# Optimization experiments

Hardware: AMD Instinct MI355X
Metric: run time of the kernel (lower is better)

Reference implementation:

```python
import jax, jax.numpy as jnp
import numpy as np

N = 65536      # nodes
E = 1048576    # edges (avg degree 16)
L = 24         # input_length == lstm input size == lstm num_layers
H = 64         # lstm hidden


def _lin_init(key, fi, fo):
    return jax.random.normal(key, (fi, fo), jnp.float32) / np.sqrt(fi)


def setup_inputs() -> dict:
    key = jax.random.key(0)
    ks = iter(jax.random.split(key, 64))
    d = {}
    d["x"] = jax.random.normal(next(ks), (N, 421 + L), jnp.float32)
    d["edge_index"] = jax.random.randint(next(ks), (2, E), 0, N)

    def lin(fi, fo):
        return _lin_init(next(ks), fi, fo), jnp.zeros((fo,), jnp.float32)

    d["poi1_W"], d["poi1_b"] = lin(13, 64)
    d["poi2_W"], d["poi2_b"] = lin(64, 64)
    d["svi1_W"], d["svi1_b"] = lin(365, 128)
    d["svi2_W"], d["svi2_b"] = lin(128, 128)
    d["all1_W"], d["all1_b"] = lin(192, 128)
    d["all2_W"], d["all2_b"] = lin(128, 128)
    for name, fi, fo in (("gat1", 128, 128), ("gat2", 128, 128), ("gat3", 128, 64)):
        d[name + "_W"], d[name + "_b"] = lin(fi, fo)
        d[name + "_asrc"] = jax.random.normal(next(ks), (fo,), jnp.float32) / np.sqrt(fo)
        d[name + "_adst"] = jax.random.normal(next(ks), (fo,), jnp.float32) / np.sqrt(fo)
    d["lstm_Wih0"] = jax.random.normal(next(ks), (L, 4 * H), jnp.float32) / np.sqrt(L)
    d["lstm_Wih"] = jax.random.normal(next(ks), (L - 1, H, 4 * H), jnp.float32) / np.sqrt(H)
    d["lstm_Whh"] = jax.random.normal(next(ks), (L, H, 4 * H), jnp.float32) / np.sqrt(H)
    d["lstm_b"] = jnp.zeros((L, 4 * H), jnp.float32)
    d["time1_W"], d["time1_b"] = lin(64, 64)
    d["time2_W"], d["time2_b"] = lin(64, 64)
    d["lin1_W"], d["lin1_b"] = lin(128, 64)
    d["lin2_W"], d["lin2_b"] = lin(64, 64)
    d["lin3_W"], d["lin3_b"] = lin(64, 1)
    return d


def _gat(h_in, W, a_src, a_dst, b, src, dst, n):
    # PyG GATConv (1 head): gather -> per-edge attn -> segment softmax -> scatter
    h = h_in @ W                                   # [N, F]
    s = h @ a_src                                  # [N]
    t = h @ a_dst                                  # [N]
    e = jax.nn.leaky_relu(s[src] + t[dst], 0.2)    # [E']
    m = jax.ops.segment_max(e, dst, num_segments=n)
    ee = jnp.exp(e - m[dst])
    denom = jax.ops.segment_sum(ee, dst, num_segments=n)
    alpha = ee / denom[dst]
    out = jax.ops.segment_sum(h[src] * alpha[:, None], dst, num_segments=n)
    return out + b


def _forward(x, poi1_W, poi1_b, poi2_W, poi2_b, svi1_W, svi1_b, svi2_W, svi2_b,
             all1_W, all1_b, all2_W, all2_b,
             gat1_W, gat1_b, gat1_asrc, gat1_adst,
             gat2_W, gat2_b, gat2_asrc, gat2_adst,
             gat3_W, gat3_b, gat3_asrc, gat3_adst,
             lstm_Wih0, lstm_Wih, lstm_Whh, lstm_b,
             time1_W, time1_b, time2_W, time2_b,
             lin1_W, lin1_b, lin2_W, lin2_b, lin3_W, lin3_b,
             edge_index):
    n = x.shape[0]
    relu = jax.nn.relu
    # feature-branch MLPs
    x_poi = relu(relu(x[:, 3:16] @ poi1_W + poi1_b) @ poi2_W + poi2_b)
    x_svi = relu(relu(x[:, 56:421] @ svi1_W + svi1_b) @ svi2_W + svi2_b)
    h = jnp.concatenate([x_poi, x_svi], axis=1)
    h = relu(relu(h @ all1_W + all1_b) @ all2_W + all2_b)
    # add self loops once (PyG GATConv default add_self_loops=True)
    loops = jnp.arange(n, dtype=edge_index.dtype)
    src = jnp.concatenate([edge_index[0], loops])
    dst = jnp.concatenate([edge_index[1], loops])
    h = relu(_gat(h, gat1_W, gat1_asrc, gat1_adst, gat1_b, src, dst, n))
    h = relu(_gat(h, gat2_W, gat2_asrc, gat2_adst, gat2_b, src, dst, n))
    h = relu(_gat(h, gat3_W, gat3_asrc, gat3_adst, gat3_b, src, dst, n))
    # stacked LSTM over the single timestep t (h0=c0=0 -> f gate & Whh contribute 0)
    inp = x[:, 421:]                               # [N, L]
    hs = []
    for l in range(L):
        Wih = lstm_Wih0 if l == 0 else lstm_Wih[l - 1]
        gates = inp @ Wih + lstm_b[l]              # [N, 4H], torch gate order i,f,g,o
        i, f, g, o = jnp.split(gates, 4, axis=-1)
        c = jax.nn.sigmoid(i) * jnp.tanh(g)
        h_l = jax.nn.sigmoid(o) * jnp.tanh(c)
        hs.append(h_l)
        inp = h_l
    t = hs[2]                                      # hn[2]
    t = relu(relu(t @ time1_W + time1_b) @ time2_W + time2_b)
    z = jnp.concatenate([h, t], axis=1)            # [N, 128]
    z = relu(z @ lin1_W + lin1_b)
    z = relu(z @ lin2_W + lin2_b)
    return z @ lin3_W + lin3_b                     # [N, 1]


def reference(x, edge_index, poi1_W, poi1_b, poi2_W, poi2_b, svi1_W, svi1_b,
              svi2_W, svi2_b, all1_W, all1_b, all2_W, all2_b,
              gat1_W, gat1_b, gat1_asrc, gat1_adst,
              gat2_W, gat2_b, gat2_asrc, gat2_adst,
              gat3_W, gat3_b, gat3_asrc, gat3_adst,
              lstm_Wih0, lstm_Wih, lstm_Whh, lstm_b,
              time1_W, time1_b, time2_W, time2_b,
              lin1_W, lin1_b, lin2_W, lin2_b, lin3_W, lin3_b):
    return _forward(x, poi1_W, poi1_b, poi2_W, poi2_b, svi1_W, svi1_b, svi2_W, svi2_b,
                    all1_W, all1_b, all2_W, all2_b,
                    gat1_W, gat1_b, gat1_asrc, gat1_adst,
                    gat2_W, gat2_b, gat2_asrc, gat2_adst,
                    gat3_W, gat3_b, gat3_asrc, gat3_adst,
                    lstm_Wih0, lstm_Wih, lstm_Whh, lstm_b,
                    time1_W, time1_b, time2_W, time2_b,
                    lin1_W, lin1_b, lin2_W, lin2_b, lin3_W, lin3_b,
                    edge_index)
```

## Files before the change

kernel.cpp:

```cpp
#include <hip/hip_runtime.h>
#include <math.h>

#define DEV __device__ __forceinline__

typedef __attribute__((ext_vector_type(8))) short short8;
typedef __attribute__((ext_vector_type(4))) float f32x4;
typedef float f32x4u __attribute__((ext_vector_type(4), aligned(4)));
typedef __attribute__((ext_vector_type(4))) unsigned int u32x4;
typedef __attribute__((ext_vector_type(4))) _Float16 h16x4;

#define NEG_BIG (-3.0e38f)
#define CAPB 4096
#define CHUNK 4096

DEV float sigm(float x) { return 1.0f / (1.0f + __expf(-x)); }
DEV float leaky(float e) { return (e >= 0.0f) ? e : 0.2f * e; }

DEV void split_bf16(const float f[8], short8& hi, short8& lo) {
#pragma unroll
  for (int i = 0; i < 8; ++i) {
    unsigned u = __builtin_bit_cast(unsigned, f[i]);
    hi[i] = (short)(u >> 16);
    float h = __builtin_bit_cast(float, u & 0xffff0000u);
    float r = f[i] - h;
    lo[i] = (short)(__builtin_bit_cast(unsigned, r) >> 16);
  }
}

DEV unsigned packsplit(float v) {
  unsigned u = __builtin_bit_cast(unsigned, v);
  unsigned hf = u & 0xffff0000u;
  float r = v - __builtin_bit_cast(float, hf);
  return hf | (__builtin_bit_cast(unsigned, r) >> 16);
}

DEV void unpack_pk(const u32x4 p0, const u32x4 p1, short8& hi, short8& lo) {
  u32x4 h, l;
  h[0] = __builtin_amdgcn_perm(p0[1], p0[0], 0x07060302u);
  h[1] = __builtin_amdgcn_perm(p0[3], p0[2], 0x07060302u);
  h[2] = __builtin_amdgcn_perm(p1[1], p1[0], 0x07060302u);
  h[3] = __builtin_amdgcn_perm(p1[3], p1[2], 0x07060302u);
  l[0] = __builtin_amdgcn_perm(p0[1], p0[0], 0x05040100u);
  l[1] = __builtin_amdgcn_perm(p0[3], p0[2], 0x05040100u);
  l[2] = __builtin_amdgcn_perm(p1[1], p1[0], 0x05040100u);
  l[3] = __builtin_amdgcn_perm(p1[3], p1[2], 0x05040100u);
  hi = __builtin_bit_cast(short8, h);
  lo = __builtin_bit_cast(short8, l);
}

template <int G, int MT, int NT>
DEV void mfma_grp(f32x4 (&acc)[MT][NT], const short8 (&ah)[MT],
                  const short8 (&al)[MT], const short8 (&bh)[4],
                  const short8 (&bl)[4]) {
#pragma unroll
  for (int mt = 0; mt < MT; ++mt)
#pragma unroll
    for (int j = 0; j < 4; ++j) {
      acc[mt][G * 4 + j] = __builtin_amdgcn_mfma_f32_16x16x32_bf16(
          ah[mt], bh[j], acc[mt][G * 4 + j], 0, 0, 0);
      acc[mt][G * 4 + j] = __builtin_amdgcn_mfma_f32_16x16x32_bf16(
          ah[mt], bl[j], acc[mt][G * 4 + j], 0, 0, 0);
      acc[mt][G * 4 + j] = __builtin_amdgcn_mfma_f32_16x16x32_bf16(
          al[mt], bh[j], acc[mt][G * 4 + j], 0, 0, 0);
    }
}


__global__ void fill_i32_kernel(int* p, int v, int n) {
  int i = blockIdx.x * blockDim.x + threadIdx.x;
  if (i < n) p[i] = v;
}


__global__ __launch_bounds__(256) void bucket_bin(
    const int* __restrict__ ei, int* __restrict__ bucket_cnt,
    unsigned* __restrict__ ebuf, int E, int Et) {
  __shared__ unsigned stage[CHUNK];
  __shared__ int hist[512], rbase[512], lcur[512];
  const int tid = threadIdx.x;
  const long long e0 = (long long)blockIdx.x * CHUNK;
  const int nalive = (int)((Et - e0) < CHUNK ? (Et - e0) : CHUNK);
  for (int i = tid; i < 512; i += 256) hist[i] = 0;
  __syncthreads();
  for (int k = tid; k < nalive; k += 256) {
    long long e = e0 + k;
    int s, d;
    if (e < E) { s = ei[e]; d = ei[E + e]; } else { s = (int)(e - E); d = s; }
    unsigned p = (unsigned)s | ((unsigned)d << 16);
    stage[k] = p;
    atomicAdd(&hist[d >> 7], 1);
  }
  __syncthreads();
  for (int i = tid; i < 512; i += 256) {
    int c = hist[i];
    rbase[i] = c ? atomicAdd(&bucket_cnt[i], c) : 0;
    lcur[i] = 0;
  }
  __syncthreads();
  for (int k = tid; k < nalive; k += 256) {
    unsigned p = stage[k];
    int b = (int)(p >> 23);
    int lofs = atomicAdd(&lcur[b], 1);
    int pos = rbase[b] + lofs;
    if (pos < CAPB) ebuf[(long long)b * CAPB + pos] = p;
  }
}

__global__ __launch_bounds__(512) void bucket_scan(
    const int* __restrict__ cnt, int* __restrict__ start, int Et) {
  __shared__ int sh[512];
  int tid = threadIdx.x;
  int v = cnt[tid];
  sh[tid] = v;
  __syncthreads();
  int val = v;
  for (int off = 1; off < 512; off <<= 1) {
    int add = (tid >= off) ? sh[tid - off] : 0;
    __syncthreads();
    val += add;
    sh[tid] = val;
    __syncthreads();
  }
  start[tid] = val - v;
  if (tid == 511) start[512] = Et;
}

__global__ __launch_bounds__(128) void bucket_csr(
    const unsigned* __restrict__ ebuf, const int* __restrict__ bucket_cnt,
    const int* __restrict__ bucket_start, int* __restrict__ row_start,
    int* __restrict__ srcs, int N, int Et) {
  __shared__ unsigned stage[CAPB];
  __shared__ int hist[128], hbase[128], lcur[128];
  const int b = blockIdx.x, tid = threadIdx.x;
  int cnt = bucket_cnt[b];
  cnt = cnt < CAPB ? cnt : CAPB;
  const int gbase = bucket_start[b];
  hist[tid] = 0;
  __syncthreads();
  const unsigned* eb = ebuf + (long long)b * CAPB;
  for (int k = tid; k < cnt; k += 128) {
    unsigned p = eb[k];
    stage[k] = p;
    atomicAdd(&hist[(p >> 16) & 127], 1);
  }
  __syncthreads();
  int v = hist[tid];
  hbase[tid] = v;
  __syncthreads();
  int val = v;
  for (int off = 1; off < 128; off <<= 1) {
    int add = (tid >= off) ? hbase[tid - off] : 0;
    __syncthreads();
    val += add;
    hbase[tid] = val;
    __syncthreads();
  }
  int ex = val - v;
  row_start[b * 128 + tid] = gbase + ex;
  __syncthreads();
  hbase[tid] = ex;
  lcur[tid] = 0;
  __syncthreads();
  for (int k = tid; k < cnt; k += 128) {
    unsigned p = stage[k];
    int o = (p >> 16) & 127;
    int lofs = atomicAdd(&lcur[o], 1);
    srcs[gbase + hbase[o] + lofs] = (int)(p & 0xffffu);
  }
  if (b == 0 && tid == 0) row_start[N] = Et;
}

struct WJobs {
  const float* W[16];
  short* hi[16];
  short* lo[16];
  int K[16];
  int M16[16];
  int ldw[16];
  int skip[16];
  int tile0[16];
};

__global__ __launch_bounds__(64) void wsplit_all(WJobs jb, int njobs) {
  int b = blockIdx.x;
  int ji = 0;
#pragma unroll
  for (int i = 1; i < 16; ++i)
    if (i < njobs && b >= jb.tile0[i]) ji = i;
  int t = b - jb.tile0[ji];
  int M16 = jb.M16[ji];
  int kc = t / M16, ntG = t % M16;
  int K = jb.K[ji], ldw = jb.ldw[ji];
  const float* __restrict__ W = jb.W[ji];

  int lane = threadIdx.x;
  int kb = kc * 32 + (lane >> 4) * 8;
  int c = ntG * 16 + (lane & 15);
  if (jb.skip[ji] && c >= 64) c += 64;
  float f[8];
#pragma unroll
  for (int j = 0; j < 8; ++j) {
    int k = kb + j;
    f[j] = (k < K) ? W[(long long)k * ldw + c] : 0.0f;
  }
  short8 h, l;
  split_bf16(f, h, l);
  long long off = ((long long)t * 64 + lane) * 8;
  *(short8*)(jb.hi[ji] + off) = h;
  *(short8*)(jb.lo[ji] + off) = l;
}


struct GemmArgs {
  const void* A; const short* wh; const short* wl; const float* bias;
  void* C; const float* asrc; const float* adst; float* sOut; float* tOut;
  int lda, ldc, K, KC, act;
};

struct LstmArgs {
  const void* A; const short* wh; const short* wl; const float* bias;
  unsigned* H; int lda, K, KC;
};

template <int MT, int NT, int APK, int OPK, int STE>
DEV void gemm_body(const GemmArgs& g, int bid) {
  const int lane = threadIdx.x;
  const int m = lane & 15, q = lane >> 4;
  const long long r0 = (long long)bid * (MT * 16);
  const int K = g.K, KC = g.KC, lda = g.lda;

  f32x4 acc[MT][NT];
#pragma unroll
  for (int i = 0; i < MT; ++i)
#pragma unroll
    for (int j = 0; j < NT; ++j) acc[i][j] = (f32x4)(0.0f);

  u32x4 pA[MT][2];
  float fA[MT][8];

  auto loadA = [&](int kc) {
#pragma unroll
    for (int mt = 0; mt < MT; ++mt) {
      if (APK == 1) {
        const unsigned* ap =
            (const unsigned*)g.A + (r0 + mt * 16 + m) * lda + kc * 32 + q * 8;
        pA[mt][0] = *(const u32x4*)ap;
        pA[mt][1] = *(const u32x4*)(ap + 4);
      } else {
        const float* ap =
            (const float*)g.A + (r0 + mt * 16 + m) * lda + kc * 32 + q * 8;
        if (kc * 32 + 32 <= K) {
          f32x4u p0 = *(const f32x4u*)ap;
          f32x4u p1 = *(const f32x4u*)(ap + 4);
#pragma unroll
          for (int j = 0; j < 4; ++j) { fA[mt][j] = p0[j]; fA[mt][4 + j] = p1[j]; }
        } else {
#pragma unroll
          for (int j = 0; j < 8; ++j) {
            int k = kc * 32 + q * 8 + j;
            fA[mt][j] = (k < K) ? ap[j] : 0.0f;
          }
        }
      }
    }
  };

  short8 ah[MT], al[MT];
  auto unpackA = [&]() {
#pragma unroll
    for (int mt = 0; mt < MT; ++mt) {
      if (APK == 1)
        unpack_pk(pA[mt][0], pA[mt][1], ah[mt], al[mt]);
      else
        split_bf16(fA[mt], ah[mt], al[mt]);
    }
  };

  short8 bh0[4], bl0[4], bh1[4], bl1[4];
  auto loadB = [&](short8 (&bh)[4], short8 (&bl)[4], int kc, int gg) {
#pragma unroll
    for (int j = 0; j < 4; ++j) {
      long long off = (((long long)kc * NT + (gg * 4 + j)) * 64 + lane) * 8;
      bh[j] = *(const short8*)(g.wh + off);
      bl[j] = *(const short8*)(g.wl + off);
    }
  };

  if constexpr (NT == 4) {
    loadA(0);
    loadB(bh0, bl0, 0, 0);
    int kc = 0;
    for (; kc + 2 <= KC; kc += 2) {
      unpackA();
      loadB(bh1, bl1, kc + 1, 0);
      loadA(kc + 1);
      mfma_grp<0, MT, NT>(acc, ah, al, bh0, bl0);
      unpackA();
      if (kc + 2 < KC) {
        loadB(bh0, bl0, kc + 2, 0);
        loadA(kc + 2);
      }
      mfma_grp<0, MT, NT>(acc, ah, al, bh1, bl1);
    }
    if (kc < KC) {
      unpackA();
      mfma_grp<0, MT, NT>(acc, ah, al, bh0, bl0);
    }
  } else {
    loadA(0);
    loadB(bh0, bl0, 0, 0);
    for (int kc = 0; kc < KC; ++kc) {
      unpackA();
      loadB(bh1, bl1, kc, 1);
      if (kc + 1 < KC) loadA(kc + 1);
      mfma_grp<0, MT, NT>(acc, ah, al, bh0, bl0);
      if (kc + 1 < KC) loadB(bh0, bl0, kc + 1, 0);
      mfma_grp<1, MT, NT>(acc, ah, al, bh1, bl1);
    }
  }

  if (STE == 2) {
    float w3[NT], bs[NT];
#pragma unroll
    for (int nt = 0; nt < NT; ++nt) {
      int col = nt * 16 + m;
      w3[nt] = g.asrc[col];
      bs[nt] = g.bias[col];
    }
#pragma unroll
    for (int mt = 0; mt < MT; ++mt)
#pragma unroll
      for (int reg = 0; reg < 4; ++reg) {
        float ps = 0.0f;
#pragma unroll
        for (int nt = 0; nt < NT; ++nt) {
          float v = fmaxf(acc[mt][nt][reg] + bs[nt], 0.0f);
          ps = fmaf(v, w3[nt], ps);
        }
#pragma unroll
        for (int off = 1; off < 16; off <<= 1) ps += __shfl_xor(ps, off, 64);
        if (m == 0) g.sOut[r0 + mt * 16 + q * 4 + reg] = ps + g.adst[0];
      }
    return;
  }

#pragma unroll
  for (int nt = 0; nt < NT; ++nt) {
    int col = nt * 16 + m;
    float bsv = g.bias ? g.bias[col] : 0.0f;
#pragma unroll
    for (int mt = 0; mt < MT; ++mt) {
      long long rb = r0 + mt * 16 + q * 4;
#pragma unroll
      for (int reg = 0; reg < 4; ++reg) {
        float v = acc[mt][nt][reg] + bsv;
        if (g.act == 1) v = fmaxf(v, 0.0f);
        if (OPK == 1)
          ((unsigned*)g.C)[(rb + reg) * g.ldc + col] = packsplit(v);
        else if (OPK == 2)
          ((_Float16*)g.C)[(rb + reg) * g.ldc + col] = (_Float16)v;
        else
          ((float*)g.C)[(rb + reg) * g.ldc + col] = v;
      }
    }
  }

  if (STE == 1) {
    float as[NT], ad[NT];
#pragma unroll
    for (int nt = 0; nt < NT; ++nt) {
      int col = nt * 16 + m;
      as[nt] = g.asrc[col];
      ad[nt] = g.adst[col];
    }
#pragma unroll
    for (int mt = 0; mt < MT; ++mt)
#pragma unroll
      for (int reg = 0; reg < 4; ++reg) {
        float ps = 0.0f, pt = 0.0f;
#pragma unroll
        for (int nt = 0; nt < NT; ++nt) {
          ps = fmaf(acc[mt][nt][reg], as[nt], ps);
          pt = fmaf(acc[mt][nt][reg], ad[nt], pt);
        }
#pragma unroll
        for (int off = 1; off < 16; off <<= 1) {
          ps += __shfl_xor(ps, off, 64);
          pt += __shfl_xor(pt, off, 64);
        }
        if (m == 0) {
          long long r = r0 + mt * 16 + q * 4 + reg;
          g.sOut[r] = ps;
          g.tOut[r] = pt;
        }
      }
  }
}

template <int APK>
DEV void lstm_body(const LstmArgs& g, int bid) {
  const int lane = threadIdx.x;
  const int m = lane & 15, q = lane >> 4;
  const long long r0 = (long long)bid * 16;
  const int K = g.K, KC = g.KC, lda = g.lda;

  f32x4 acc[12];
#pragma unroll
  for (int j = 0; j < 12; ++j) acc[j] = (f32x4)(0.0f);

  u32x4 pA[2];
  float fA[8];

  auto loadA = [&](int kc) {
    if (APK == 1) {
      const unsigned* ap = (const unsigned*)g.A + (r0 + m) * lda + kc * 32 + q * 8;
      pA[0] = *(const u32x4*)ap;
      pA[1] = *(const u32x4*)(ap + 4);
    } else {
      const float* ap = (const float*)g.A + (r0 + m) * lda + kc * 32 + q * 8;
      if (kc * 32 + 32 <= K) {
        f32x4u p0 = *(const f32x4u*)ap;
        f32x4u p1 = *(const f32x4u*)(ap + 4);
#pragma unroll
        for (int j = 0; j < 4; ++j) { fA[j] = p0[j]; fA[4 + j] = p1[j]; }
      } else {
#pragma unroll
        for (int j = 0; j < 8; ++j) {
          int k = kc * 32 + q * 8 + j;
          fA[j] = (k < K) ? ap[j] : 0.0f;
        }
      }
    }
  };

  short8 bh0, bl0, bh1, bl1;
  auto loadB = [&](short8& bh, short8& bl, int kc, int nt) {
    long long off = (((long long)kc * 12 + nt) * 64 + lane) * 8;
    bh = *(const short8*)(g.wh + off);
    bl = *(const short8*)(g.wl + off);
  };

  loadA(0);
  loadB(bh0, bl0, 0, 0);
  for (int kc = 0; kc < KC; ++kc) {
    short8 ah, al;
    if (APK == 1)
      unpack_pk(pA[0], pA[1], ah, al);
    else
      split_bf16(fA, ah, al);
    loadB(bh1, bl1, kc, 1);
    if (kc + 1 < KC) loadA(kc + 1);
    const int kn = (kc + 1 < KC) ? kc + 1 : kc;
#pragma unroll
    for (int nt = 0; nt < 12; ++nt) {
      short8& cbh = (nt & 1) ? bh1 : bh0;
      short8& cbl = (nt & 1) ? bl1 : bl0;
      acc[nt] = __builtin_amdgcn_mfma_f32_16x16x32_bf16(ah, cbh, acc[nt], 0, 0, 0);
      acc[nt] = __builtin_amdgcn_mfma_f32_16x16x32_bf16(ah, cbl, acc[nt], 0, 0, 0);
      acc[nt] = __builtin_amdgcn_mfma_f32_16x16x32_bf16(al, cbh, acc[nt], 0, 0, 0);
      if (nt + 2 < 12)
        loadB((nt & 1) ? bh1 : bh0, (nt & 1) ? bl1 : bl0, kc, nt + 2);
      else if (nt + 2 == 12)
        loadB(bh0, bl0, kn, 0);
    }
  }

#pragma unroll
  for (int nt = 0; nt < 4; ++nt) {
    int col = nt * 16 + m;
    float bi = g.bias[col], bg = g.bias[128 + col], bo = g.bias[192 + col];
#pragma unroll
    for (int reg = 0; reg < 4; ++reg) {
      float gi = acc[nt][reg] + bi;
      float gg = acc[nt + 4][reg] + bg;
      float go = acc[nt + 8][reg] + bo;
      float cc = sigm(gi) * tanhf(gg);
      g.H[(r0 + q * 4 + reg) * 64 + col] = packsplit(sigm(go) * tanhf(cc));
    }
  }
}


template <int MT, int NT, int APK, int OPK, int STE>
__global__ __launch_bounds__(64) void gemm_mfma(GemmArgs g) {
  gemm_body<MT, NT, APK, OPK, STE>(g, blockIdx.x);
}

template <int NTa, int APKa, int OPKa, int STEa,
          int NTb, int APKb, int OPKb, int STEb>
__global__ __launch_bounds__(64) void combo_gg(GemmArgs a, GemmArgs b, int nA) {
  int bid = blockIdx.x;
  if (bid < nA)
    gemm_body<2, NTa, APKa, OPKa, STEa>(a, bid);
  else
    gemm_body<2, NTb, APKb, OPKb, STEb>(b, bid - nA);
}

template <int NTa, int APKa, int OPKa, int STEa, int LAPK>
__global__ __launch_bounds__(64) void combo_gl(GemmArgs a, LstmArgs l, int nA) {
  int bid = blockIdx.x;
  if (bid < nA)
    gemm_body<2, NTa, APKa, OPKa, STEa>(a, bid);
  else
    lstm_body<LAPK>(l, bid - nA);
}

template <int NTa, int APKa, int OPKa, int STEa,
          int NTb, int APKb, int OPKb, int STEb, int LAPK>
__global__ __launch_bounds__(64) void combo_ggl(GemmArgs a, GemmArgs b,
                                                LstmArgs l, int nA, int nAB) {
  int bid = blockIdx.x;
  if (bid < nA)
    gemm_body<2, NTa, APKa, OPKa, STEa>(a, bid);
  else if (bid < nAB)
    gemm_body<2, NTb, APKb, OPKb, STEb>(b, bid - nA);
  else
    lstm_body<LAPK>(l, bid - nAB);
}


template <int FO, int OPK>
__global__ __launch_bounds__(256) void gat_agg(
    const _Float16* __restrict__ G, const float* __restrict__ s,
    const float* __restrict__ t, const int* __restrict__ row_start,
    const int* __restrict__ srcs, const float* __restrict__ bias,
    void* __restrict__ outv, int ldc) {
  constexpr int CAP = 128;
  constexpr int LPE = FO / 4;
  constexpr int EPW = 64 / LPE;
  __shared__ float ecache[4][CAP];
  __shared__ int icache[4][CAP];
  const int wv = threadIdx.x >> 6;
  const int lane = threadIdx.x & 63;
  const int d = blockIdx.x * 4 + wv;
  const int start = row_start[d], end = row_start[d + 1];
  const float td = t[d];

  float m = NEG_BIG, dsum = 0.0f;
  for (int j = start + lane; j < end; j += 64) {
    int sj = srcs[j];
    float e = leaky(s[sj] + td);
    int idx = j - start;
    if (idx < CAP) { ecache[wv][idx] = e; icache[wv][idx] = sj; }
    float mn = fmaxf(m, e);
    dsum = dsum * __expf(m - mn) + __expf(e - mn);
    m = mn;
  }
#pragma unroll
  for (int off = 32; off; off >>= 1) {
    float mo = __shfl_xor(m, off, 64);
    float dso = __shfl_xor(dsum, off, 64);
    float mn = fmaxf(m, mo);
    dsum = dsum * __expf(m - mn) + dso * __expf(mo - mn);
    m = mn;
  }
  const float inv = 1.0f / dsum;

  const int deg = end - start;
  const int capdeg = deg < CAP ? deg : CAP;
  for (int idx = lane; idx < capdeg; idx += 64)
    ecache[wv][idx] = __expf(ecache[wv][idx] - m) * inv;
  __syncthreads();

  const int grp = lane / LPE, cl = lane % LPE;
  const _Float16* __restrict__ Gc = G + cl * 4;
  float a0 = 0.0f, a1 = 0.0f, a2 = 0.0f, a3 = 0.0f;
  int idx = grp;
  for (; idx + 3 * EPW < capdeg; idx += 4 * EPW) {
    const int i1 = idx + EPW, i2 = idx + 2 * EPW, i3 = idx + 3 * EPW;
    int s0 = icache[wv][idx], s1 = icache[wv][i1];
    int s2 = icache[wv][i2], s3 = icache[wv][i3];
    float l0 = ecache[wv][idx], l1 = ecache[wv][i1];
    float l2 = ecache[wv][i2], l3 = ecache[wv][i3];
    h16x4 g0 = *(const h16x4*)(Gc + (long long)s0 * FO);
    h16x4 g1 = *(const h16x4*)(Gc + (long long)s1 * FO);
    h16x4 g2 = *(const h16x4*)(Gc + (long long)s2 * FO);
    h16x4 g3 = *(const h16x4*)(Gc + (long long)s3 * FO);
    a0 = fmaf(l0, (float)g0[0], a0); a1 = fmaf(l0, (float)g0[1], a1);
    a2 = fmaf(l0, (float)g0[2], a2); a3 = fmaf(l0, (float)g0[3], a3);
    a0 = fmaf(l1, (float)g1[0], a0); a1 = fmaf(l1, (float)g1[1], a1);
    a2 = fmaf(l1, (float)g1[2], a2); a3 = fmaf(l1, (float)g1[3], a3);
    a0 = fmaf(l2, (float)g2[0], a0); a1 = fmaf(l2, (float)g2[1], a1);
    a2 = fmaf(l2, (float)g2[2], a2); a3 = fmaf(l2, (float)g2[3], a3);
    a0 = fmaf(l3, (float)g3[0], a0); a1 = fmaf(l3, (float)g3[1], a1);
    a2 = fmaf(l3, (float)g3[2], a2); a3 = fmaf(l3, (float)g3[3], a3);
  }
  for (; idx + EPW < capdeg; idx += 2 * EPW) {
    const int i1 = idx + EPW;
    int s0 = icache[wv][idx], s1 = icache[wv][i1];
    float l0 = ecache[wv][idx], l1 = ecache[wv][i1];
    h16x4 g0 = *(const h16x4*)(Gc + (long long)s0 * FO);
    h16x4 g1 = *(const h16x4*)(Gc + (long long)s1 * FO);
    a0 = fmaf(l0, (float)g0[0], a0); a1 = fmaf(l0, (float)g0[1], a1);
    a2 = fmaf(l0, (float)g0[2], a2); a3 = fmaf(l0, (float)g0[3], a3);
    a0 = fmaf(l1, (float)g1[0], a0); a1 = fmaf(l1, (float)g1[1], a1);
    a2 = fmaf(l1, (float)g1[2], a2); a3 = fmaf(l1, (float)g1[3], a3);
  }
  for (; idx < capdeg; idx += EPW) {
    int s0 = icache[wv][idx];
    float l0 = ecache[wv][idx];
    h16x4 g0 = *(const h16x4*)(Gc + (long long)s0 * FO);
    a0 = fmaf(l0, (float)g0[0], a0); a1 = fmaf(l0, (float)g0[1], a1);
    a2 = fmaf(l0, (float)g0[2], a2); a3 = fmaf(l0, (float)g0[3], a3);
  }
  for (; idx < deg; idx += EPW) {
    int s0 = srcs[start + idx];
    float l0 = __expf(leaky(s[s0] + td) - m) * inv;
    h16x4 g0 = *(const h16x4*)(Gc + (long long)s0 * FO);
    a0 = fmaf(l0, (float)g0[0], a0); a1 = fmaf(l0, (float)g0[1], a1);
    a2 = fmaf(l0, (float)g0[2], a2); a3 = fmaf(l0, (float)g0[3], a3);
  }
#pragma unroll
  for (int off = 32; off >= LPE; off >>= 1) {
    a0 += __shfl_xor(a0, off, 64);
    a1 += __shfl_xor(a1, off, 64);
    a2 += __shfl_xor(a2, off, 64);
    a3 += __shfl_xor(a3, off, 64);
  }
  if (grp == 0) {
    f32x4u bs = *(const f32x4u*)(bias + cl * 4);
    float v0 = fmaxf(a0 + bs[0], 0.0f);
    float v1 = fmaxf(a1 + bs[1], 0.0f);
    float v2 = fmaxf(a2 + bs[2], 0.0f);
    float v3 = fmaxf(a3 + bs[3], 0.0f);
    if (OPK == 1) {
      u32x4 pv;
      pv[0] = packsplit(v0); pv[1] = packsplit(v1);
      pv[2] = packsplit(v2); pv[3] = packsplit(v3);
      *(u32x4*)((unsigned*)outv + (long long)d * ldc + cl * 4) = pv;
    } else {
      f32x4u v; v[0] = v0; v[1] = v1; v[2] = v2; v[3] = v3;
      *(f32x4u*)((float*)outv + (long long)d * ldc + cl * 4) = v;
    }
  }
}


struct WSplit { const short* hi; const short* lo; };

extern "C" void kernel_launch(void* const* d_in, const int* in_sizes, int n_in,
                              void* d_out, int out_size, void* d_ws, size_t ws_size,
                              hipStream_t stream) {
  const int N = 65536, E = 1048576;
  const int Et = E + N;

  const float* x        = (const float*)d_in[0];
  const int*   ei       = (const int*)d_in[1];
  const float* poi1_W   = (const float*)d_in[2];
  const float* poi1_b   = (const float*)d_in[3];
  const float* poi2_W   = (const float*)d_in[4];
  const float* poi2_b   = (const float*)d_in[5];
  const float* svi1_W   = (const float*)d_in[6];
  const float* svi1_b   = (const float*)d_in[7];
  const float* svi2_W   = (const float*)d_in[8];
  const float* svi2_b   = (const float*)d_in[9];
  const float* all1_W   = (const float*)d_in[10];
  const float* all1_b   = (const float*)d_in[11];
  const float* all2_W   = (const float*)d_in[12];
  const float* all2_b   = (const float*)d_in[13];
  const float* gat1_W   = (const float*)d_in[14];
  const float* gat1_b   = (const float*)d_in[15];
  const float* gat1_as  = (const float*)d_in[16];
  const float* gat1_ad  = (const float*)d_in[17];
  const float* gat2_W   = (const float*)d_in[18];
  const float* gat2_b   = (const float*)d_in[19];
  const float* gat2_as  = (const float*)d_in[20];
  const float* gat2_ad  = (const float*)d_in[21];
  const float* gat3_W   = (const float*)d_in[22];
  const float* gat3_b   = (const float*)d_in[23];
  const float* gat3_as  = (const float*)d_in[24];
  const float* gat3_ad  = (const float*)d_in[25];
  const float* lstm_Wih0= (const float*)d_in[26];
  const float* lstm_Wih = (const float*)d_in[27];
  const float* lstm_b   = (const float*)d_in[29];
  const float* time1_W  = (const float*)d_in[30];
  const float* time1_b  = (const float*)d_in[31];
  const float* time2_W  = (const float*)d_in[32];
  const float* time2_b  = (const float*)d_in[33];
  const float* lin1_W   = (const float*)d_in[34];
  const float* lin1_b   = (const float*)d_in[35];
  const float* lin2_W   = (const float*)d_in[36];
  const float* lin2_b   = (const float*)d_in[37];
  const float* lin3_W   = (const float*)d_in[38];
  const float* lin3_b   = (const float*)d_in[39];
  float* out = (float*)d_out;

  float* wsf   = (float*)d_ws;
  float* R192  = wsf;
  float* RA    = R192 + (size_t)N * 192;
  float* RB    = RA + (size_t)N * 128;
  float* Rz    = RB + (size_t)N * 128;
  float* LA    = Rz + (size_t)N * 128;
  float* LB    = LA + (size_t)N * 64;
  float* sArr  = LB + (size_t)N * 64;
  float* tArr  = sArr + N;
  int* ints         = (int*)(tArr + N);
  int* row_start    = ints;
  int* srcs         = row_start + (N + 1);
  int* bucket_cnt   = srcs + Et;
  int* bucket_start = bucket_cnt + 512;
  unsigned* ebuf    = (unsigned*)(bucket_start + 513);
  short* pool = (short*)(((uintptr_t)(ebuf + 512 * CAPB) + 15) & ~(uintptr_t)15);

  WJobs jb{};
  int nj = 0, tiles = 0;
  auto split = [&](const float* W, int K, int M, int ldw, int skip) -> WSplit {
    int KC = (K + 31) / 32;
    size_t sz = (size_t)KC * M * 32;
    short* hi = pool; pool += sz;
    short* lo = pool; pool += sz;
    jb.W[nj] = W; jb.hi[nj] = hi; jb.lo[nj] = lo;
    jb.K[nj] = K; jb.M16[nj] = M / 16; jb.ldw[nj] = ldw; jb.skip[nj] = skip;
    jb.tile0[nj] = tiles;
    tiles += KC * (M / 16);
    ++nj;
    return {hi, lo};
  };

  auto mkg = [&](const void* A, int lda, WSplit w, const float* bias, void* C,
                 int ldc, int K, int act, const float* as_ = nullptr,
                 const float* ad_ = nullptr, float* sO = nullptr,
                 float* tO = nullptr) -> GemmArgs {
    GemmArgs g;
    g.A = A; g.lda = lda; g.wh = w.hi; g.wl = w.lo; g.bias = bias;
    g.C = C; g.ldc = ldc; g.K = K; g.KC = (K + 31) / 32; g.act = act;
    g.asrc = as_; g.adst = ad_; g.sOut = sO; g.tOut = tO;
    return g;
  };
  auto mkl = [&](const void* A, int lda, WSplit w, const float* bias,
                 unsigned* H, int K) -> LstmArgs {
    LstmArgs l;
    l.A = A; l.lda = lda; l.wh = w.hi; l.wl = w.lo; l.bias = bias;
    l.H = H; l.K = K; l.KC = (K + 31) / 32;
    return l;
  };

  WSplit wpoi1 = split(poi1_W, 13, 64, 64, 0);
  WSplit wpoi2 = split(poi2_W, 64, 64, 64, 0);
  WSplit wsvi1 = split(svi1_W, 365, 128, 128, 0);
  WSplit wsvi2 = split(svi2_W, 128, 128, 128, 0);
  WSplit wall1 = split(all1_W, 192, 128, 128, 0);
  WSplit wall2 = split(all2_W, 128, 128, 128, 0);
  WSplit wg1   = split(gat1_W, 128, 128, 128, 0);
  WSplit wg2   = split(gat2_W, 128, 128, 128, 0);
  WSplit wg3   = split(gat3_W, 128, 64, 64, 0);
  WSplit wls0  = split(lstm_Wih0, 24, 192, 256, 1);
  WSplit wls1  = split(lstm_Wih, 64, 192, 256, 1);
  WSplit wls2  = split(lstm_Wih + 64 * 256, 64, 192, 256, 1);
  WSplit wt1   = split(time1_W, 64, 64, 64, 0);
  WSplit wt2   = split(time2_W, 64, 64, 64, 0);
  WSplit wl1   = split(lin1_W, 128, 64, 64, 0);
  WSplit wl2   = split(lin2_W, 64, 64, 64, 0);
  hipLaunchKernelGGL(wsplit_all, dim3(tiles), dim3(64), 0, stream, jb, nj);

  const int TB = 256;
  const int GB = N / 32;
  const int LBK = N / 16;

  hipLaunchKernelGGL(fill_i32_kernel, dim3(2), dim3(TB), 0, stream,
                     bucket_cnt, 0, 512);
  hipLaunchKernelGGL(bucket_bin, dim3((Et + CHUNK - 1) / CHUNK), dim3(256),
                     0, stream, ei, bucket_cnt, ebuf, E, Et);
  hipLaunchKernelGGL(bucket_scan, dim3(1), dim3(512), 0, stream,
                     bucket_cnt, bucket_start, Et);
  hipLaunchKernelGGL(bucket_csr, dim3(512), dim3(128), 0, stream,
                     ebuf, bucket_cnt, bucket_start, row_start, srcs, N, Et);

  _Float16* Gh = (_Float16*)RA;

  hipLaunchKernelGGL((combo_ggl<8, 0, 1, 0, 4, 0, 1, 0, 0>),
                     dim3(GB + GB + LBK), dim3(64), 0, stream,
                     mkg(x + 56, 445, wsvi1, svi1_b, RB, 128, 365, 1),
                     mkg(x + 3, 445, wpoi1, poi1_b, RA, 64, 13, 1),
                     mkl(x + 421, 445, wls0, lstm_b, (unsigned*)LA, 24),
                     GB, GB + GB);
  hipLaunchKernelGGL((combo_ggl<8, 1, 1, 0, 4, 1, 1, 0, 1>),
                     dim3(GB + GB + LBK), dim3(64), 0, stream,
                     mkg(RB, 128, wsvi2, svi2_b, R192 + 64, 192, 128, 1),
                     mkg(RA, 64, wpoi2, poi2_b, R192, 192, 64, 1),
                     mkl(LA, 64, wls1, lstm_b + 256, (unsigned*)LB, 64),
                     GB, GB + GB);
  hipLaunchKernelGGL((combo_gl<8, 1, 1, 0, 1>),
                     dim3(GB + LBK), dim3(64), 0, stream,
                     mkg(R192, 192, wall1, all1_b, RA, 128, 192, 1),
                     mkl(LB, 64, wls2, lstm_b + 512, (unsigned*)LA, 64), GB);
  hipLaunchKernelGGL((combo_gg<8, 1, 1, 0, 4, 1, 1, 0>),
                     dim3(GB + GB), dim3(64), 0, stream,
                     mkg(RA, 128, wall2, all2_b, RB, 128, 128, 1),
                     mkg(LA, 64, wt1, time1_b, LB, 64, 64, 1), GB);
  hipLaunchKernelGGL((combo_gg<8, 1, 2, 1, 4, 1, 1, 0>),
                     dim3(GB + GB), dim3(64), 0, stream,
                     mkg(RB, 128, wg1, nullptr, Gh, 128, 128, 0,
                         gat1_as, gat1_ad, sArr, tArr),
                     mkg(LB, 64, wt2, time2_b, Rz + 64, 128, 64, 1), GB);

  const int aggBlocks = N / 4;

  hipLaunchKernelGGL((gat_agg<128, 1>), dim3(aggBlocks), dim3(256), 0, stream,
                     Gh, sArr, tArr, row_start, srcs, gat1_b, RB, 128);
  hipLaunchKernelGGL((gemm_mfma<2, 8, 1, 2, 1>), dim3(GB), dim3(64), 0, stream,
                     mkg(RB, 128, wg2, nullptr, Gh, 128, 128, 0,
                         gat2_as, gat2_ad, sArr, tArr));
  hipLaunchKernelGGL((gat_agg<128, 1>), dim3(aggBlocks), dim3(256), 0, stream,
                     Gh, sArr, tArr, row_start, srcs, gat2_b, RB, 128);
  hipLaunchKernelGGL((gemm_mfma<2, 4, 1, 2, 1>), dim3(GB), dim3(64), 0, stream,
                     mkg(RB, 128, wg3, nullptr, Gh, 64, 128, 0,
                         gat3_as, gat3_ad, sArr, tArr));
  hipLaunchKernelGGL((gat_agg<64, 1>), dim3(aggBlocks), dim3(256), 0, stream,
                     Gh, sArr, tArr, row_start, srcs, gat3_b, Rz, 128);

  hipLaunchKernelGGL((gemm_mfma<2, 4, 1, 1, 0>), dim3(GB), dim3(64), 0, stream,
                     mkg(Rz, 128, wl1, lin1_b, RA, 64, 128, 1));
  hipLaunchKernelGGL((gemm_mfma<2, 4, 1, 0, 2>), dim3(GB), dim3(64), 0, stream,
                     mkg(RA, 64, wl2, lin2_b, nullptr, 64, 64, 2,
                         lin3_W, lin3_b, out, nullptr));
}
```

Measured before the change: 648.5 us.

## Fuse consecutive dense layers per tile through LDS to cut launches and global traffic

Chains of dense layers (svi1→svi2, poi1→poi2, the three LSTM layers plus both time layers, all1→all2, lin1→lin2→lin3) now run inside one block each. Intermediate activations are staged in shared memory in packed split-bf16 form instead of being written to and read back from global buffers. The original five combo launches for the towers collapse into one tower kernel plus one pair kernel, and the head GEMMs become a single kernel. This removes several launches and large intermediate global round-trips, at the cost of LDS use per 64-thread block, which may reduce occupancy and serialise work inside longer-running blocks.

```diff
diff --git a/kernel.cpp b/kernel.cpp
--- a/kernel.cpp
+++ b/kernel.cpp
@@ -211,25 +211,12 @@
 }
 
 
-struct GemmArgs {
-  const void* A; const short* wh; const short* wl; const float* bias;
-  void* C; const float* asrc; const float* adst; float* sOut; float* tOut;
-  int lda, ldc, K, KC, act;
-};
-
-struct LstmArgs {
-  const void* A; const short* wh; const short* wl; const float* bias;
-  unsigned* H; int lda, K, KC;
-};
-
-template <int MT, int NT, int APK, int OPK, int STE>
-DEV void gemm_body(const GemmArgs& g, int bid) {
+template <int MT, int NT, int APK>
+DEV void gemm_loop(const void* __restrict__ Av, long long abase, int lda,
+                   const short* __restrict__ wh, const short* __restrict__ wl,
+                   int K, int KC, f32x4 (&acc)[MT][NT]) {
   const int lane = threadIdx.x;
   const int m = lane & 15, q = lane >> 4;
-  const long long r0 = (long long)bid * (MT * 16);
-  const int K = g.K, KC = g.KC, lda = g.lda;
-
-  f32x4 acc[MT][NT];
 #pragma unroll
   for (int i = 0; i < MT; ++i)
 #pragma unroll
@@ -243,12 +230,12 @@
     for (int mt = 0; mt < MT; ++mt) {
       if (APK == 1) {
         const unsigned* ap =
-            (const unsigned*)g.A + (r0 + mt * 16 + m) * lda + kc * 32 + q * 8;
+            (const unsigned*)Av + (abase + mt * 16 + m) * lda + kc * 32 + q * 8;
         pA[mt][0] = *(const u32x4*)ap;
         pA[mt][1] = *(const u32x4*)(ap + 4);
       } else {
         const float* ap =
-            (const float*)g.A + (r0 + mt * 16 + m) * lda + kc * 32 + q * 8;
+            (const float*)Av + (abase + mt * 16 + m) * lda + kc * 32 + q * 8;
         if (kc * 32 + 32 <= K) {
           f32x4u p0 = *(const f32x4u*)ap;
           f32x4u p1 = *(const f32x4u*)(ap + 4);
@@ -281,8 +268,8 @@
 #pragma unroll
     for (int j = 0; j < 4; ++j) {
       long long off = (((long long)kc * NT + (gg * 4 + j)) * 64 + lane) * 8;
-      bh[j] = *(const short8*)(g.wh + off);
-      bl[j] = *(const short8*)(g.wl + off);
+      bh[j] = *(const short8*)(wh + off);
+      bl[j] = *(const short8*)(wl + off);
     }
   };
 
@@ -318,31 +305,63 @@
       mfma_grp<1, MT, NT>(acc, ah, al, bh1, bl1);
     }
   }
-
-  if (STE == 2) {
-    float w3[NT], bs[NT];
-#pragma unroll
-    for (int nt = 0; nt < NT; ++nt) {
-      int col = nt * 16 + m;
-      w3[nt] = g.asrc[col];
-      bs[nt] = g.bias[col];
-    }
+}
+
+
+template <int MT, int NT>
+DEV void epi_packed(const f32x4 (&acc)[MT][NT], const float* bias,
+                    unsigned* C, int ldc, long long r0, int act) {
+  const int lane = threadIdx.x;
+  const int m = lane & 15, q = lane >> 4;
+#pragma unroll
+  for (int nt = 0; nt < NT; ++nt) {
+    int col = nt * 16 + m;
+    float b = bias ? bias[col] : 0.0f;
+#pragma unroll
+    for (int mt = 0; mt < MT; ++mt) {
+      long long rb = r0 + mt * 16 + q * 4;
+#pragma unroll
+      for (int reg = 0; reg < 4; ++reg) {
+        float v = acc[mt][nt][reg] + b;
+        if (act) v = fmaxf(v, 0.0f);
+        C[(rb + reg) * ldc + col] = packsplit(v);
+      }
+    }
+  }
+}
+
+template <int MT, int NT>
+DEV void epi_lds(const f32x4 (&acc)[MT][NT], const float* bias,
+                 unsigned* L, int S) {
+  const int lane = threadIdx.x;
+  const int m = lane & 15, q = lane >> 4;
+#pragma unroll
+  for (int nt = 0; nt < NT; ++nt) {
+    int col = nt * 16 + m;
+    float b = bias[col];
 #pragma unroll
     for (int mt = 0; mt < MT; ++mt)
 #pragma unroll
       for (int reg = 0; reg < 4; ++reg) {
-        float ps = 0.0f;
-#pragma unroll
-        for (int nt = 0; nt < NT; ++nt) {
-          float v = fmaxf(acc[mt][nt][reg] + bs[nt], 0.0f);
-          ps = fmaf(v, w3[nt], ps);
-        }
-#pragma unroll
-        for (int off = 1; off < 16; off <<= 1) ps += __shfl_xor(ps, off, 64);
-        if (m == 0) g.sOut[r0 + mt * 16 + q * 4 + reg] = ps + g.adst[0];
+        float v = fmaxf(acc[mt][nt][reg] + b, 0.0f);
+        L[(mt * 16 + q * 4 + reg) * S + col] = packsplit(v);
       }
-    return;
-  }
+  }
+}
+
+struct GemmArgs {
+  const void* A; const short* wh; const short* wl; const float* bias;
+  void* C; const float* asrc; const float* adst; float* sOut; float* tOut;
+  int lda, ldc, K, KC, act;
+};
+
+template <int MT, int NT, int APK, int OPK, int STE>
+__global__ __launch_bounds__(64) void gemm_mfma(GemmArgs g) {
+  const int lane = threadIdx.x;
+  const int m = lane & 15, q = lane >> 4;
+  const long long r0 = (long long)blockIdx.x * (MT * 16);
+  f32x4 acc[MT][NT];
+  gemm_loop<MT, NT, APK>(g.A, r0, g.lda, g.wh, g.wl, g.K, g.KC, acc);
 
 #pragma unroll
   for (int nt = 0; nt < NT; ++nt) {
@@ -397,14 +416,54 @@
   }
 }
 
+
+struct PairJob {
+  const void* A; int lda, K1;
+  const short *w1h, *w1l; const float* b1;
+  const short *w2h, *w2l; const float* b2; int K2;
+  unsigned* C; int ldc;
+};
+
+template <int NT1, int APK1, int NT2>
+DEV void pair_body(const PairJob& j, int bid, unsigned* lbuf) {
+  constexpr int S = NT1 * 16 + 4;
+  const long long r0 = (long long)bid * 32;
+  {
+    f32x4 acc[2][NT1];
+    gemm_loop<2, NT1, APK1>(j.A, r0, j.lda, j.w1h, j.w1l, j.K1,
+                            (j.K1 + 31) / 32, acc);
+    epi_lds<2, NT1>(acc, j.b1, lbuf, S);
+  }
+  {
+    f32x4 acc[2][NT2];
+    gemm_loop<2, NT2, 1>(lbuf, 0, S, j.w2h, j.w2l, j.K2, (j.K2 + 31) / 32, acc);
+    epi_packed<2, NT2>(acc, j.b2, j.C, j.ldc, r0, 1);
+  }
+}
+
+template <int NT1, int APK1, int NT2>
+__global__ __launch_bounds__(64) void pair_kernel(PairJob j) {
+  __shared__ __align__(16) unsigned lbuf[32 * 132];
+  pair_body<NT1, APK1, NT2>(j, blockIdx.x, lbuf);
+}
+
+
+struct ChainJob {
+  const float* x; int lda;
+  const short *w0h, *w0l; const float* b0;
+  const short *w1h, *w1l; const float* b1;
+  const short *w2h, *w2l; const float* b2;
+  const short *t1h, *t1l; const float* tb1;
+  const short *t2h, *t2l; const float* tb2;
+  unsigned* C; int ldc;
+};
+
 template <int APK>
-DEV void lstm_body(const LstmArgs& g, int bid) {
+DEV void lstm_loop(const void* __restrict__ Av, long long abase, int lda,
+                   const short* __restrict__ wh, const short* __restrict__ wl,
+                   int K, int KC, f32x4 (&acc)[12]) {
   const int lane = threadIdx.x;
   const int m = lane & 15, q = lane >> 4;
-  const long long r0 = (long long)bid * 16;
-  const int K = g.K, KC = g.KC, lda = g.lda;
-
-  f32x4 acc[12];
 #pragma unroll
   for (int j = 0; j < 12; ++j) acc[j] = (f32x4)(0.0f);
 
@@ -413,11 +472,12 @@
 
   auto loadA = [&](int kc) {
     if (APK == 1) {
-      const unsigned* ap = (const unsigned*)g.A + (r0 + m) * lda + kc * 32 + q * 8;
+      const unsigned* ap =
+          (const unsigned*)Av + (abase + m) * lda + kc * 32 + q * 8;
       pA[0] = *(const u32x4*)ap;
       pA[1] = *(const u32x4*)(ap + 4);
     } else {
-      const float* ap = (const float*)g.A + (r0 + m) * lda + kc * 32 + q * 8;
+      const float* ap = (const float*)Av + (abase + m) * lda + kc * 32 + q * 8;
       if (kc * 32 + 32 <= K) {
         f32x4u p0 = *(const f32x4u*)ap;
         f32x4u p1 = *(const f32x4u*)(ap + 4);
@@ -436,8 +496,8 @@
   short8 bh0, bl0, bh1, bl1;
   auto loadB = [&](short8& bh, short8& bl, int kc, int nt) {
     long long off = (((long long)kc * 12 + nt) * 64 + lane) * 8;
-    bh = *(const short8*)(g.wh + off);
-    bl = *(const short8*)(g.wl + off);
+    bh = *(const short8*)(wh + off);
+    bl = *(const short8*)(wl + off);
   };
 
   loadA(0);
@@ -464,58 +524,116 @@
         loadB(bh0, bl0, kn, 0);
     }
   }
-
+}
+
+DEV void lstm_epi_lds(const f32x4 (&acc)[12], const float* bias,
+                      unsigned* L, int S) {
+  const int lane = threadIdx.x;
+  const int m = lane & 15, q = lane >> 4;
 #pragma unroll
   for (int nt = 0; nt < 4; ++nt) {
     int col = nt * 16 + m;
-    float bi = g.bias[col], bg = g.bias[128 + col], bo = g.bias[192 + col];
+    float bi = bias[col], bg = bias[128 + col], bo = bias[192 + col];
 #pragma unroll
     for (int reg = 0; reg < 4; ++reg) {
       float gi = acc[nt][reg] + bi;
       float gg = acc[nt + 4][reg] + bg;
       float go = acc[nt + 8][reg] + bo;
       float cc = sigm(gi) * tanhf(gg);
-      g.H[(r0 + q * 4 + reg) * 64 + col] = packsplit(sigm(go) * tanhf(cc));
-    }
-  }
-}
-
-
-template <int MT, int NT, int APK, int OPK, int STE>
-__global__ __launch_bounds__(64) void gemm_mfma(GemmArgs g) {
-  gemm_body<MT, NT, APK, OPK, STE>(g, blockIdx.x);
-}
-
-template <int NTa, int APKa, int OPKa, int STEa,
-          int NTb, int APKb, int OPKb, int STEb>
-__global__ __launch_bounds__(64) void combo_gg(GemmArgs a, GemmArgs b, int nA) {
+      L[(q * 4 + reg) * S + col] = packsplit(sigm(go) * tanhf(cc));
+    }
+  }
+}
+
+DEV void chain_body(const ChainJob& c, int bid, unsigned* lbuf) {
+  constexpr int S = 68;
+  const long long r0 = (long long)bid * 16;
+  unsigned* H0 = lbuf;
+  unsigned* H1 = lbuf + 16 * S;
+  {
+    f32x4 acc[12];
+    lstm_loop<0>(c.x, r0, c.lda, c.w0h, c.w0l, 24, 1, acc);
+    lstm_epi_lds(acc, c.b0, H0, S);
+  }
+  {
+    f32x4 acc[12];
+    lstm_loop<1>(H0, 0, S, c.w1h, c.w1l, 64, 2, acc);
+    lstm_epi_lds(acc, c.b1, H1, S);
+  }
+  {
+    f32x4 acc[12];
+    lstm_loop<1>(H1, 0, S, c.w2h, c.w2l, 64, 2, acc);
+    lstm_epi_lds(acc, c.b2, H0, S);
+  }
+  {
+    f32x4 acc[1][4];
+    gemm_loop<1, 4, 1>(H0, 0, S, c.t1h, c.t1l, 64, 2, acc);
+    epi_lds<1, 4>(acc, c.tb1, H1, S);
+  }
+  {
+    f32x4 acc[1][4];
+    gemm_loop<1, 4, 1>(H1, 0, S, c.t2h, c.t2l, 64, 2, acc);
+    epi_packed<1, 4>(acc, c.tb2, c.C, c.ldc, r0, 1);
+  }
+}
+
+
+__global__ __launch_bounds__(64) void tower_combo(PairJob svi, PairJob poi,
+                                                  ChainJob ch, int nA, int nAB) {
+  __shared__ __align__(16) unsigned lbuf[32 * 132];
   int bid = blockIdx.x;
   if (bid < nA)
-    gemm_body<2, NTa, APKa, OPKa, STEa>(a, bid);
+    pair_body<8, 0, 8>(svi, bid, lbuf);
+  else if (bid < nAB)
+    pair_body<4, 0, 4>(poi, bid - nA, lbuf);
   else
-    gemm_body<2, NTb, APKb, OPKb, STEb>(b, bid - nA);
-}
-
-template <int NTa, int APKa, int OPKa, int STEa, int LAPK>
-__global__ __launch_bounds__(64) void combo_gl(GemmArgs a, LstmArgs l, int nA) {
-  int bid = blockIdx.x;
-  if (bid < nA)
-    gemm_body<2, NTa, APKa, OPKa, STEa>(a, bid);
-  else
-    lstm_body<LAPK>(l, bid - nA);
-}
-
-template <int NTa, int APKa, int OPKa, int STEa,
-          int NTb, int APKb, int OPKb, int STEb, int LAPK>
-__global__ __launch_bounds__(64) void combo_ggl(GemmArgs a, GemmArgs b,
-                                                LstmArgs l, int nA, int nAB) {
-  int bid = blockIdx.x;
-  if (bid < nA)
-    gemm_body<2, NTa, APKa, OPKa, STEa>(a, bid);
-  else if (bid < nAB)
-    gemm_body<2, NTb, APKb, OPKb, STEb>(b, bid - nA);
-  else
-    lstm_body<LAPK>(l, bid - nAB);
+    chain_body(ch, bid - nAB, lbuf);
+}
+
+
+struct HeadJob {
+  const void* A; int lda, K1;
+  const short *w1h, *w1l; const float* b1;
+  const short *w2h, *w2l; const float* b2; int K2;
+  const float* w3; const float* b3; float* out;
+};
+
+__global__ __launch_bounds__(64) void head_kernel(HeadJob j) {
+  __shared__ __align__(16) unsigned lbuf[32 * 68];
+  constexpr int S = 68;
+  const int lane = threadIdx.x;
+  const int m = lane & 15, q = lane >> 4;
+  const long long r0 = (long long)blockIdx.x * 32;
+  {
+    f32x4 acc[2][4];
+    gemm_loop<2, 4, 1>(j.A, r0, j.lda, j.w1h, j.w1l, j.K1, (j.K1 + 31) / 32, acc);
+    epi_lds<2, 4>(acc, j.b1, lbuf, S);
+  }
+  {
+    f32x4 acc[2][4];
+    gemm_loop<2, 4, 1>(lbuf, 0, S, j.w2h, j.w2l, j.K2, (j.K2 + 31) / 32, acc);
+    float w3[4], bs[4];
+#pragma unroll
+    for (int nt = 0; nt < 4; ++nt) {
+      int col = nt * 16 + m;
+      w3[nt] = j.w3[col];
+      bs[nt] = j.b2[col];
+    }
+#pragma unroll
+    for (int mt = 0; mt < 2; ++mt)
+#pragma unroll
+      for (int reg = 0; reg < 4; ++reg) {
+        float ps = 0.0f;
+#pragma unroll
+        for (int nt = 0; nt < 4; ++nt) {
+          float v = fmaxf(acc[mt][nt][reg] + bs[nt], 0.0f);
+          ps = fmaf(v, w3[nt], ps);
+        }
+#pragma unroll
+        for (int off = 1; off < 16; off <<= 1) ps += __shfl_xor(ps, off, 64);
+        if (m == 0) j.out[r0 + mt * 16 + q * 4 + reg] = ps + j.b3[0];
+      }
+  }
 }
 
 
@@ -690,9 +808,7 @@
   float* RA    = R192 + (size_t)N * 192;
   float* RB    = RA + (size_t)N * 128;
   float* Rz    = RB + (size_t)N * 128;
-  float* LA    = Rz + (size_t)N * 128;
-  float* LB    = LA + (size_t)N * 64;
-  float* sArr  = LB + (size_t)N * 64;
+  float* sArr  = Rz + (size_t)N * 128;
   float* tArr  = sArr + N;
   int* ints         = (int*)(tArr + N);
   int* row_start    = ints;
@@ -726,13 +842,6 @@
     g.C = C; g.ldc = ldc; g.K = K; g.KC = (K + 31) / 32; g.act = act;
     g.asrc = as_; g.adst = ad_; g.sOut = sO; g.tOut = tO;
     return g;
-  };
-  auto mkl = [&](const void* A, int lda, WSplit w, const float* bias,
-                 unsigned* H, int K) -> LstmArgs {
-    LstmArgs l;
-    l.A = A; l.lda = lda; l.wh = w.hi; l.wl = w.lo; l.bias = bias;
-    l.H = H; l.K = K; l.KC = (K + 31) / 32;
-    return l;
   };
 
   WSplit wpoi1 = split(poi1_W, 13, 64, 64, 0);
@@ -755,7 +864,7 @@
 
   const int TB = 256;
   const int GB = N / 32;
-  const int LBK = N / 16;
+  const int CB = N / 16;
 
   hipLaunchKernelGGL(fill_i32_kernel, dim3(2), dim3(TB), 0, stream,
                      bucket_cnt, 0, 512);
@@ -768,34 +877,40 @@
 
   _Float16* Gh = (_Float16*)RA;
 
-  hipLaunchKernelGGL((combo_ggl<8, 0, 1, 0, 4, 0, 1, 0, 0>),
-                     dim3(GB + GB + LBK), dim3(64), 0, stream,
-                     mkg(x + 56, 445, wsvi1, svi1_b, RB, 128, 365, 1),
-                     mkg(x + 3, 445, wpoi1, poi1_b, RA, 64, 13, 1),
-                     mkl(x + 421, 445, wls0, lstm_b, (unsigned*)LA, 24),
-                     GB, GB + GB);
-  hipLaunchKernelGGL((combo_ggl<8, 1, 1, 0, 4, 1, 1, 0, 1>),
-                     dim3(GB + GB + LBK), dim3(64), 0, stream,
-                     mkg(RB, 128, wsvi2, svi2_b, R192 + 64, 192, 128, 1),
-                     mkg(RA, 64, wpoi2, poi2_b, R192, 192, 64, 1),
-                     mkl(LA, 64, wls1, lstm_b + 256, (unsigned*)LB, 64),
-                     GB, GB + GB);
-  hipLaunchKernelGGL((combo_gl<8, 1, 1, 0, 1>),
-                     dim3(GB + LBK), dim3(64), 0, stream,
-                     mkg(R192, 192, wall1, all1_b, RA, 128, 192, 1),
-                     mkl(LB, 64, wls2, lstm_b + 512, (unsigned*)LA, 64), GB);
-  hipLaunchKernelGGL((combo_gg<8, 1, 1, 0, 4, 1, 1, 0>),
-                     dim3(GB + GB), dim3(64), 0, stream,
-                     mkg(RA, 128, wall2, all2_b, RB, 128, 128, 1),
-                     mkg(LA, 64, wt1, time1_b, LB, 64, 64, 1), GB);
-  hipLaunchKernelGGL((combo_gg<8, 1, 2, 1, 4, 1, 1, 0>),
-                     dim3(GB + GB), dim3(64), 0, stream,
+  PairJob svi;
+  svi.A = x + 56; svi.lda = 445; svi.K1 = 365;
+  svi.w1h = wsvi1.hi; svi.w1l = wsvi1.lo; svi.b1 = svi1_b;
+  svi.w2h = wsvi2.hi; svi.w2l = wsvi2.lo; svi.b2 = svi2_b; svi.K2 = 128;
+  svi.C = (unsigned*)R192 + 64; svi.ldc = 192;
+  PairJob poi;
+  poi.A = x + 3; poi.lda = 445; poi.K1 = 13;
+  poi.w1h = wpoi1.hi; poi.w1l = wpoi1.lo; poi.b1 = poi1_b;
+  poi.w2h = wpoi2.hi; poi.w2l = wpoi2.lo; poi.b2 = poi2_b; poi.K2 = 64;
+  poi.C = (unsigned*)R192; poi.ldc = 192;
+  ChainJob ch;
+  ch.x = x + 421; ch.lda = 445;
+  ch.w0h = wls0.hi; ch.w0l = wls0.lo; ch.b0 = lstm_b;
+  ch.w1h = wls1.hi; ch.w1l = wls1.lo; ch.b1 = lstm_b + 256;
+  ch.w2h = wls2.hi; ch.w2l = wls2.lo; ch.b2 = lstm_b + 512;
+  ch.t1h = wt1.hi; ch.t1l = wt1.lo; ch.tb1 = time1_b;
+  ch.t2h = wt2.hi; ch.t2l = wt2.lo; ch.tb2 = time2_b;
+  ch.C = (unsigned*)Rz + 64; ch.ldc = 128;
+  hipLaunchKernelGGL(tower_combo, dim3(GB + GB + CB), dim3(64), 0, stream,
+                     svi, poi, ch, GB, GB + GB);
+
+  PairJob allp;
+  allp.A = R192; allp.lda = 192; allp.K1 = 192;
+  allp.w1h = wall1.hi; allp.w1l = wall1.lo; allp.b1 = all1_b;
+  allp.w2h = wall2.hi; allp.w2l = wall2.lo; allp.b2 = all2_b; allp.K2 = 128;
+  allp.C = (unsigned*)RB; allp.ldc = 128;
+  hipLaunchKernelGGL((pair_kernel<8, 1, 8>), dim3(GB), dim3(64), 0, stream,
+                     allp);
+
+  const int aggBlocks = N / 4;
+
+  hipLaunchKernelGGL((gemm_mfma<2, 8, 1, 2, 1>), dim3(GB), dim3(64), 0, stream,
                      mkg(RB, 128, wg1, nullptr, Gh, 128, 128, 0,
-                         gat1_as, gat1_ad, sArr, tArr),
-                     mkg(LB, 64, wt2, time2_b, Rz + 64, 128, 64, 1), GB);
-
-  const int aggBlocks = N / 4;
-
+                         gat1_as, gat1_ad, sArr, tArr));
   hipLaunchKernelGGL((gat_agg<128, 1>), dim3(aggBlocks), dim3(256), 0, stream,
                      Gh, sArr, tArr, row_start, srcs, gat1_b, RB, 128);
   hipLaunchKernelGGL((gemm_mfma<2, 8, 1, 2, 1>), dim3(GB), dim3(64), 0, stream,
@@ -809,9 +924,10 @@
   hipLaunchKernelGGL((gat_agg<64, 1>), dim3(aggBlocks), dim3(256), 0, stream,
                      Gh, sArr, tArr, row_start, srcs, gat3_b, Rz, 128);
 
-  hipLaunchKernelGGL((gemm_mfma<2, 4, 1, 1, 0>), dim3(GB), dim3(64), 0, stream,
-                     mkg(Rz, 128, wl1, lin1_b, RA, 64, 128, 1));
-  hipLaunchKernelGGL((gemm_mfma<2, 4, 1, 0, 2>), dim3(GB), dim3(64), 0, stream,
-                     mkg(RA, 64, wl2, lin2_b, nullptr, 64, 64, 2,
-                         lin3_W, lin3_b, out, nullptr));
-}
+  HeadJob hd;
+  hd.A = Rz; hd.lda = 128; hd.K1 = 128;
+  hd.w1h = wl1.hi; hd.w1l = wl1.lo; hd.b1 = lin1_b;
+  hd.w2h = wl2.hi; hd.w2l = wl2.lo; hd.b2 = lin2_b; hd.K2 = 64;
+  hd.w3 = lin3_W; hd.b3 = lin3_b; hd.out = out;
+  hipLaunchKernelGGL(head_kernel, dim3(GB), dim3(64), 0, stream, hd);
+}
```

New measurement: 583.0 us. -10.1%, faster.
